# Optimization experiments

Measured on AMD Instinct MI355X. Metric: run time of the kernel, lower is better.

## Reference

```python
import jax, jax.numpy as jnp
import numpy as np

H = 12           # num_heads
D_MODEL = 768
SCALE = (D_MODEL // H) ** -0.5  # qk_scale default: head_dim**-0.5


def _attn_mask(q, k, v, mask):
    # sim: (b, i, j); mask broadcast over query dim (mask.unsqueeze(1) in torch)
    sim = jnp.einsum('bid,bjd->bij', q, k) + mask[:, None, :]
    a = jax.nn.softmax(sim, axis=-1)
    return jnp.einsum('bij,bjd->bid', a, v)


def setup_inputs() -> dict:
    key = jax.random.key(0)
    k0, k1, k2, k3 = jax.random.split(key, 4)
    B, F, n, D = 16, 8, 196, 768
    N = 1 + F * n  # cls + frames*patches = 1569
    x = jax.random.normal(k0, (B, N, D), jnp.float32)
    x_mask = jax.random.normal(k1, (B, N), jnp.float32)  # additive attention mask
    Wqkv = jax.random.normal(k2, (3 * D, D), jnp.float32) * (D ** -0.5)
    Wproj = jax.random.normal(k3, (D, D), jnp.float32) * (D ** -0.5)
    bproj = jnp.zeros((D,), jnp.float32)
    return {"x": x, "x_mask": x_mask, "Wqkv": Wqkv, "Wproj": Wproj,
            "bproj": bproj, "f": F}


def reference(x, x_mask, Wqkv, Wproj, bproj, f):
    B, N, D = x.shape
    h = H
    d = D // h
    # qkv projection (qkv_bias=False), split into q,k,v
    qkv = x @ Wqkv.T                       # (B, N, 3D)
    q, k, v = jnp.split(qkv, 3, axis=-1)

    def to_heads(t):  # 'b n (h d) -> (b h) n d'
        return t.reshape(B, N, h, d).transpose(0, 2, 1, 3).reshape(B * h, N, d)

    q, k, v = map(to_heads, (q, k, v))
    mask = jnp.repeat(x_mask, h, axis=0)   # repeat_interleave over heads: (B*h, N)

    q = q * SCALE
    cls_q, q_ = q[:, :1], q[:, 1:]
    cls_k, k_ = k[:, :1], k[:, 1:]
    cls_v, v_ = v[:, :1], v[:, 1:]
    cls_mask, mask_ = mask[:, :1], mask[:, 1:]

    # cls token attends to everything
    cls_out = _attn_mask(cls_q, k, v, mask)            # (B*h, 1, d)

    # spatial attention: 'b (f n) d -> (b f) n d'
    n = (N - 1) // f
    q_ = q_.reshape(B * h * f, n, d)
    k_ = k_.reshape(B * h * f, n, d)
    v_ = v_.reshape(B * h * f, n, d)
    mask_ = mask_.reshape(B * h * f, n)

    # prepend cls k/v/mask to every frame group (r = f)
    cls_k = jnp.repeat(cls_k, f, axis=0)               # (B*h*f, 1, d)
    cls_v = jnp.repeat(cls_v, f, axis=0)
    cls_m = jnp.repeat(cls_mask, f, axis=0)            # (B*h*f, 1)
    k_ = jnp.concatenate([cls_k, k_], axis=1)          # (B*h*f, n+1, d)
    v_ = jnp.concatenate([cls_v, v_], axis=1)
    m2 = jnp.concatenate([cls_m, mask_], axis=1)       # (B*h*f, n+1)

    out = _attn_mask(q_, k_, v_, m2)                   # (B*h*f, n, d)
    out = out.reshape(B * h, f * n, d)                 # '(b f) n d -> b (f n) d'
    out = jnp.concatenate([cls_out, out], axis=1)      # (B*h, N, d)
    out = out.reshape(B, h, N, d).transpose(0, 2, 1, 3).reshape(B, N, D)
    return out @ Wproj.T + bproj
```

## Files before the change

kernel.cpp:

```cpp
#include <hip/hip_runtime.h>
#include <hip/hip_bf16.h>
#include <stdint.h>

#define Hh 12
#define Dm 768
#define Bb 16
#define Nt 1569
#define Ff 8
#define NC 196
#define BH 192
#define Mr 25104
#define CPW 224
#define VTW (8*CPW)
#define PLD 232
#define CLD 132

typedef __attribute__((ext_vector_type(8))) short bf16x8;
typedef __attribute__((ext_vector_type(4))) float f32x4;

typedef const __attribute__((address_space(1))) uint32_t guint;
typedef __attribute__((address_space(3))) uint32_t luint;

static __device__ __forceinline__ float bf2f(unsigned short u) {
  union { unsigned int i; float f; } v; v.i = ((unsigned int)u) << 16; return v.f;
}
static __device__ __forceinline__ unsigned short f2bf(float f) {
  __hip_bfloat16 h = __float2bfloat16(f);
  return __builtin_bit_cast(unsigned short, h);
}

__global__ void cast_bf16_k(const float4* __restrict__ src, ushort4* __restrict__ dst, int n4) {
  for (int i = blockIdx.x * blockDim.x + threadIdx.x; i < n4; i += gridDim.x * blockDim.x) {
    float4 f = src[i];
    ushort4 u;
    u.x = f2bf(f.x); u.y = f2bf(f.y); u.z = f2bf(f.z); u.w = f2bf(f.w);
    dst[i] = u;
  }
}

template<int MODE>
__global__ __launch_bounds__(256) void gemm_k(
    const __hip_bfloat16* __restrict__ A,
    const __hip_bfloat16* __restrict__ W,
    int M, int K,
    __hip_bfloat16* __restrict__ qh, __hip_bfloat16* __restrict__ kh,
    __hip_bfloat16* __restrict__ vT, __hip_bfloat16* __restrict__ vcls,
    const float* __restrict__ bias, float* __restrict__ outp)
{
  __shared__ __align__(16) unsigned short shmem[128 * CLD];
  unsigned short* ls0 = shmem;
  unsigned short* ls1 = shmem + 4096;
  unsigned short* ls2 = shmem + 8192;
  unsigned short* ls3 = shmem + 12288;

  const int tid = threadIdx.x;
  const int lane = tid & 63, wid = tid >> 6;
  const int waveM = wid >> 1, waveN = wid & 1;

  const int gridN = gridDim.x;
  const int nwg = gridDim.x * gridDim.y;
  int bid = blockIdx.y * gridN + blockIdx.x;
  int q8 = nwg >> 3, r8 = nwg & 7;
  int xcd = bid & 7, lid = bid >> 3;
  int swz = (xcd < r8 ? xcd * (q8 + 1) : r8 * (q8 + 1) + (xcd - r8) * q8) + lid;
  const int mBase = (swz / gridN) * 128, nBase = (swz % gridN) * 128;

  const int l15 = lane & 15, lg = lane >> 4;
  f32x4 acc[4][4] = {};
  const int nkt = K >> 6;
  for (int kt = 0; kt < nkt; ++kt) {
#pragma unroll
    for (int s = 0; s < 2; ++s) {
      int seg = s * 256 + tid;
      int row = seg >> 2, ks = seg & 3;
      int arow = mBase + row; if (arow >= M) arow = M - 1;
      int brow = nBase + row;
      const __hip_bfloat16* ap = A + (size_t)arow * K + kt * 64 + ks * 8;
      const __hip_bfloat16* wp = W + (size_t)brow * K + kt * 64 + ks * 8;
      __builtin_amdgcn_global_load_lds((guint*)ap,        (luint*)&ls0[seg * 8], 16, 0, 0);
      __builtin_amdgcn_global_load_lds((guint*)wp,        (luint*)&ls1[seg * 8], 16, 0, 0);
      __builtin_amdgcn_global_load_lds((guint*)(ap + 32), (luint*)&ls2[seg * 8], 16, 0, 0);
      __builtin_amdgcn_global_load_lds((guint*)(wp + 32), (luint*)&ls3[seg * 8], 16, 0, 0);
    }
    __syncthreads();
    bf16x8 aF[4], bF[4], aG[4], bG[4];
#pragma unroll
    for (int i = 0; i < 4; ++i) {
      int ro = (waveM * 64 + i * 16 + l15) * 32 + lg * 8;
      int co = (waveN * 64 + i * 16 + l15) * 32 + lg * 8;
      aF[i] = *reinterpret_cast<const bf16x8*>(&ls0[ro]);
      bF[i] = *reinterpret_cast<const bf16x8*>(&ls1[co]);
      aG[i] = *reinterpret_cast<const bf16x8*>(&ls2[ro]);
      bG[i] = *reinterpret_cast<const bf16x8*>(&ls3[co]);
    }
#pragma unroll
    for (int mi = 0; mi < 4; ++mi)
#pragma unroll
      for (int ni = 0; ni < 4; ++ni) {
        acc[mi][ni] = __builtin_amdgcn_mfma_f32_16x16x32_bf16(aF[mi], bF[ni], acc[mi][ni], 0, 0, 0);
        acc[mi][ni] = __builtin_amdgcn_mfma_f32_16x16x32_bf16(aG[mi], bG[ni], acc[mi][ni], 0, 0, 0);
      }
    __syncthreads();
  }

  if (MODE == 1) {
    const bool fullM = (mBase + 128 <= M);
#pragma unroll
    for (int mi = 0; mi < 4; ++mi)
#pragma unroll
      for (int ni = 0; ni < 4; ++ni)
#pragma unroll
        for (int r = 0; r < 4; ++r) {
          int grow = mBase + waveM * 64 + mi * 16 + lg * 4 + r;
          if (!fullM && grow >= M) continue;
          int gcol = nBase + waveN * 64 + ni * 16 + l15;
          outp[(size_t)grow * Dm + gcol] = acc[mi][ni][r] + bias[gcol];
        }
    return;
  }

  const int which = nBase / Dm;
  const int headBase = (nBase - which * Dm) >> 6;
  const float scl = (which == 0) ? 0.125f : 1.f;
  const bool fullM = (mBase + 128 <= M);

  if (fullM) {
    if (which < 2) {
#pragma unroll
      for (int mi = 0; mi < 4; ++mi)
#pragma unroll
        for (int ni = 0; ni < 4; ++ni)
#pragma unroll
          for (int r = 0; r < 4; ++r)
            shmem[(waveM * 64 + mi * 16 + lg * 4 + r) * CLD + (waveN * 64 + ni * 16 + l15)]
                = f2bf(acc[mi][ni][r] * scl);
      __syncthreads();
      __hip_bfloat16* dst = (which == 0) ? qh : kh;
      int row = tid >> 1, h = tid & 1;
      int grow = mBase + row;
      int b = grow / Nt, i = grow - b * Nt;
      const uint2* sp = reinterpret_cast<const uint2*>(&shmem[row * CLD + h * 64]);
      uint2* dp = reinterpret_cast<uint2*>(
          dst + ((size_t)(b * Hh + headBase + h) * Nt + i) * 64);
#pragma unroll
      for (int j = 0; j < 16; ++j) dp[j] = sp[j];
    } else {
#pragma unroll
      for (int mi = 0; mi < 4; ++mi)
#pragma unroll
        for (int ni = 0; ni < 4; ++ni)
#pragma unroll
          for (int r = 0; r < 4; ++r)
            shmem[(waveN * 64 + ni * 16 + l15) * CLD + (waveM * 64 + mi * 16 + lg * 4 + r)]
                = f2bf(acc[mi][ni][r]);
      __syncthreads();
      int lc = tid & 127, rhalf = tid >> 7;
      int h = lc >> 6, dc = lc & 63;
      int head = headBase + h;
#pragma unroll
      for (int g = 0; g < 8; ++g) {
        int row0 = rhalf * 64 + g * 8;
        int grow0 = mBase + row0;
        int b = grow0 / Nt, i0 = grow0 - b * Nt;
        const unsigned short* sp = &shmem[lc * CLD + row0];
        if (i0 >= 1 && i0 + 8 <= Nt) {
          int j0 = i0 - 1, cc = j0 / NC, key = j0 - cc * NC;
          if (key + 8 <= NC) {
            int bh = b * Hh + head;
            __hip_bfloat16* p = vT + ((size_t)bh * 64 + dc) * VTW + cc * CPW + key;
            if ((key & 1) == 0) {
              const unsigned int* s4 = reinterpret_cast<const unsigned int*>(sp);
              unsigned int* d4 = reinterpret_cast<unsigned int*>(p);
              d4[0] = s4[0]; d4[1] = s4[1]; d4[2] = s4[2]; d4[3] = s4[3];
            } else {
#pragma unroll
              for (int j = 0; j < 8; ++j)
                p[j] = __builtin_bit_cast(__hip_bfloat16, sp[j]);
            }
            continue;
          }
        }
#pragma unroll
        for (int j = 0; j < 8; ++j) {
          int grow = grow0 + j;
          int bb = grow / Nt, ii = grow - bb * Nt;
          int bh2 = bb * Hh + head;
          unsigned short val = sp[j];
          if (ii == 0) {
            vcls[bh2 * 64 + dc] = __builtin_bit_cast(__hip_bfloat16, val);
          } else {
            int jj = ii - 1, cc2 = jj / NC, k2 = jj - cc2 * NC;
            vT[((size_t)bh2 * 64 + dc) * VTW + cc2 * CPW + k2]
                = __builtin_bit_cast(__hip_bfloat16, val);
          }
        }
      }
    }
  } else {
#pragma unroll
    for (int mi = 0; mi < 4; ++mi)
#pragma unroll
      for (int ni = 0; ni < 4; ++ni)
#pragma unroll
        for (int r = 0; r < 4; ++r) {
          int grow = mBase + waveM * 64 + mi * 16 + lg * 4 + r;
          if (grow >= M) continue;
          int gcol = nBase + waveN * 64 + ni * 16 + l15;
          float v = acc[mi][ni][r];
          int b = grow / Nt, i = grow - b * Nt;
          int hcol = gcol - which * Dm;
          int head = hcol >> 6, dc = hcol & 63;
          int bh = b * Hh + head;
          if (which == 0) {
            qh[((size_t)bh * Nt + i) * 64 + dc] = __float2bfloat16(v * 0.125f);
          } else if (which == 1) {
            kh[((size_t)bh * Nt + i) * 64 + dc] = __float2bfloat16(v);
          } else {
            if (i == 0) vcls[bh * 64 + dc] = __float2bfloat16(v);
            else {
              int j = i - 1; int cc = j / NC, key = j - cc * NC;
              vT[((size_t)bh * 64 + dc) * VTW + cc * CPW + key] = __float2bfloat16(v);
            }
          }
        }
  }
}

__global__ __launch_bounds__(256) void cls_attn_k(
    const __hip_bfloat16* __restrict__ qh, const __hip_bfloat16* __restrict__ kh,
    const __hip_bfloat16* __restrict__ vT, const __hip_bfloat16* __restrict__ vcls,
    const float* __restrict__ x_mask, __hip_bfloat16* __restrict__ ao)
{
  const int bh = blockIdx.x, b = bh / Hh, head = bh - b * Hh;
  const int tid = threadIdx.x;
  __shared__ float sS[Nt];
  __shared__ float qv[64];
  __shared__ float red[256];
  if (tid < 64) qv[tid] = __bfloat162float(qh[((size_t)bh * Nt) * 64 + tid]);
  __syncthreads();
  float lmax = -1e30f;
  for (int j = tid; j < Nt; j += 256) {
    const __hip_bfloat16* kr = kh + ((size_t)bh * Nt + j) * 64;
    float dot = 0.f;
#pragma unroll
    for (int d0 = 0; d0 < 64; d0 += 8) {
      bf16x8 kv = *reinterpret_cast<const bf16x8*>(kr + d0);
#pragma unroll
      for (int i = 0; i < 8; ++i) dot += qv[d0 + i] * bf2f((unsigned short)kv[i]);
    }
    float s = dot + x_mask[b * Nt + j];
    sS[j] = s;
    lmax = fmaxf(lmax, s);
  }
  red[tid] = lmax; __syncthreads();
  for (int off = 128; off > 0; off >>= 1) {
    if (tid < off) red[tid] = fmaxf(red[tid], red[tid + off]);
    __syncthreads();
  }
  float m = red[0]; __syncthreads();
  float lsum = 0.f;
  for (int j = tid; j < Nt; j += 256) { float e = __expf(sS[j] - m); sS[j] = e; lsum += e; }
  red[tid] = lsum; __syncthreads();
  for (int off = 128; off > 0; off >>= 1) {
    if (tid < off) red[tid] += red[tid + off];
    __syncthreads();
  }
  float rden = 1.f / red[0]; __syncthreads();
  int dc = tid & 63, part = tid >> 6;
  float partial = 0.f;
  if (part == 0) partial = sS[0] * __bfloat162float(vcls[bh * 64 + dc]);
  const __hip_bfloat16* vrow = vT + ((size_t)bh * 64 + dc) * VTW;
  for (int cc = part * 2; cc < part * 2 + 2; ++cc) {
    int base = 1 + cc * NC;
    const __hip_bfloat16* vc2 = vrow + cc * CPW;
    int key = 0;
    for (; key + 8 <= NC; key += 8) {
      bf16x8 vv = *reinterpret_cast<const bf16x8*>(vc2 + key);
#pragma unroll
      for (int i = 0; i < 8; ++i)
        partial += sS[base + key + i] * bf2f((unsigned short)vv[i]);
    }
    for (; key < NC; ++key)
      partial += sS[base + key] * __bfloat162float(vc2[key]);
  }
  red[tid] = partial; __syncthreads();
  if (tid < 64) {
    float o = (red[tid] + red[tid + 64] + red[tid + 128] + red[tid + 192]) * rden;
    ao[((size_t)b * Nt) * Dm + head * 64 + dc] = __float2bfloat16(o);
  }
}

__global__ __launch_bounds__(64, 4) void chunk_attn_k(
    const __hip_bfloat16* __restrict__ qh, const __hip_bfloat16* __restrict__ kh,
    const __hip_bfloat16* __restrict__ vT, const __hip_bfloat16* __restrict__ vcls,
    const float* __restrict__ x_mask, __hip_bfloat16* __restrict__ ao)
{
  const int bid = blockIdx.x;
  const int work = (bid & 7) * 2496 + (bid >> 3);
  const int g = work / 13;
  const int rtile = work - g * 13;
  const int bh = g >> 3, c = g & 7;
  const int b = bh / Hh, head = bh - b * Hh;
  const int lane = threadIdx.x;
  const int l15 = lane & 15, lg = lane >> 4;
  __shared__ __align__(16) __hip_bfloat16 ldsP[16 * PLD];

  int qlrow = rtile * 16 + l15;
  int qtok = 1 + c * NC + qlrow; if (qtok > Nt - 1) qtok = Nt - 1;
  const __hip_bfloat16* qp = qh + ((size_t)bh * Nt + qtok) * 64;
  bf16x8 aQ0 = *reinterpret_cast<const bf16x8*>(qp + lg * 8);
  bf16x8 aQ1 = *reinterpret_cast<const bf16x8*>(qp + 32 + lg * 8);

  float pc0;
  {
    const __hip_bfloat16* kc = kh + (size_t)bh * Nt * 64;
    bf16x8 ck0 = *reinterpret_cast<const bf16x8*>(kc + lg * 8);
    bf16x8 ck1 = *reinterpret_cast<const bf16x8*>(kc + 32 + lg * 8);
    float p = 0.f;
#pragma unroll
    for (int i = 0; i < 8; ++i)
      p += bf2f((unsigned short)aQ0[i]) * bf2f((unsigned short)ck0[i])
         + bf2f((unsigned short)aQ1[i]) * bf2f((unsigned short)ck1[i]);
    p += __shfl_xor(p, 16);
    p += __shfl_xor(p, 32);
    pc0 = p + x_mask[b * Nt];
  }

  f32x4 S[13];
#pragma unroll 2
  for (int nt = 0; nt < 13; ++nt) {
    int key = nt * 16 + l15;
    int ktok = 1 + c * NC + key; if (ktok > Nt - 1) ktok = Nt - 1;
    const __hip_bfloat16* kp = kh + ((size_t)bh * Nt + ktok) * 64;
    bf16x8 b0 = *reinterpret_cast<const bf16x8*>(kp + lg * 8);
    bf16x8 b1 = *reinterpret_cast<const bf16x8*>(kp + 32 + lg * 8);
    f32x4 sa = {};
    sa = __builtin_amdgcn_mfma_f32_16x16x32_bf16(aQ0, b0, sa, 0, 0, 0);
    sa = __builtin_amdgcn_mfma_f32_16x16x32_bf16(aQ1, b1, sa, 0, 0, 0);
    float mv = (key < NC) ? x_mask[b * Nt + 1 + c * NC + key] : -1e30f;
#pragma unroll
    for (int r = 0; r < 4; ++r) S[nt][r] = sa[r] + mv;
  }

  float pcls[4], rden[4];
#pragma unroll
  for (int r = 0; r < 4; ++r) {
    float m = -1e30f;
#pragma unroll
    for (int nt = 0; nt < 13; ++nt) m = fmaxf(m, S[nt][r]);
    m = fmaxf(m, __shfl_xor(m, 1));
    m = fmaxf(m, __shfl_xor(m, 2));
    m = fmaxf(m, __shfl_xor(m, 4));
    m = fmaxf(m, __shfl_xor(m, 8));
    float sc = __shfl(pc0, lg * 4 + r);
    m = fmaxf(m, sc);
    float sum = 0.f;
#pragma unroll
    for (int nt = 0; nt < 13; ++nt) { float e = __expf(S[nt][r] - m); S[nt][r] = e; sum += e; }
    sum += __shfl_xor(sum, 1);
    sum += __shfl_xor(sum, 2);
    sum += __shfl_xor(sum, 4);
    sum += __shfl_xor(sum, 8);
    float pc = __expf(sc - m);
    pcls[r] = pc;
    rden[r] = 1.f / (sum + pc);
  }

#pragma unroll
  for (int nt = 0; nt < 13; ++nt)
#pragma unroll
    for (int r = 0; r < 4; ++r)
      ldsP[(lg * 4 + r) * PLD + nt * 16 + l15] = __float2bfloat16(S[nt][r]);
#pragma unroll
  for (int r = 0; r < 4; ++r)
    ldsP[l15 * PLD + 208 + lg * 4 + r] = __float2bfloat16(0.f);
  __syncthreads();

  f32x4 O[4] = {};
#pragma unroll
  for (int kt = 0; kt < 7; ++kt) {
    bf16x8 aP = *reinterpret_cast<const bf16x8*>(&ldsP[l15 * PLD + kt * 32 + lg * 8]);
#pragma unroll
    for (int ni = 0; ni < 4; ++ni) {
      int dc = ni * 16 + l15;
      bf16x8 bV = *reinterpret_cast<const bf16x8*>(
          vT + ((size_t)bh * 64 + dc) * VTW + c * CPW + kt * 32 + lg * 8);
      O[ni] = __builtin_amdgcn_mfma_f32_16x16x32_bf16(aP, bV, O[ni], 0, 0, 0);
    }
  }
#pragma unroll
  for (int ni = 0; ni < 4; ++ni) {
    int dc = ni * 16 + l15;
    float vc = __bfloat162float(vcls[bh * 64 + dc]);
#pragma unroll
    for (int r = 0; r < 4; ++r) {
      int lrow = rtile * 16 + lg * 4 + r;
      if (lrow < NC) {
        float o = (O[ni][r] + pcls[r] * vc) * rden[r];
        int tok = 1 + c * NC + lrow;
        ao[((size_t)b * Nt + tok) * Dm + head * 64 + dc] = __float2bfloat16(o);
      }
    }
  }
}

extern "C" void kernel_launch(void* const* d_in, const int* in_sizes, int n_in,
                              void* d_out, int out_size, void* d_ws, size_t ws_size,
                              hipStream_t stream) {
  const float* x     = (const float*)d_in[0];
  const float* xmask = (const float*)d_in[1];
  const float* wqkv  = (const float*)d_in[2];
  const float* wproj = (const float*)d_in[3];
  const float* bproj = (const float*)d_in[4];
  float* outp = (float*)d_out;

  char* ws = (char*)d_ws;
  size_t off = 0;
  auto alloc = [&](size_t bytes) {
    char* p = ws + off;
    off += (bytes + 255) & ~(size_t)255;
    return p;
  };
  __hip_bfloat16* xb     = (__hip_bfloat16*)alloc((size_t)Mr * Dm * 2);
  __hip_bfloat16* wqkvb  = (__hip_bfloat16*)alloc((size_t)3 * Dm * Dm * 2);
  __hip_bfloat16* wprojb = (__hip_bfloat16*)alloc((size_t)Dm * Dm * 2);
  __hip_bfloat16* qh     = (__hip_bfloat16*)alloc((size_t)BH * Nt * 64 * 2);
  __hip_bfloat16* kh     = (__hip_bfloat16*)alloc((size_t)BH * Nt * 64 * 2);
  __hip_bfloat16* vT     = (__hip_bfloat16*)alloc((size_t)BH * 64 * VTW * 2);
  __hip_bfloat16* vcls   = (__hip_bfloat16*)alloc((size_t)BH * 64 * 2);
  __hip_bfloat16* ao = xb;

  cast_bf16_k<<<2048, 256, 0, stream>>>((const float4*)x, (ushort4*)xb, Mr * Dm / 4);
  cast_bf16_k<<<512, 256, 0, stream>>>((const float4*)wqkv, (ushort4*)wqkvb, 3 * Dm * Dm / 4);
  cast_bf16_k<<<256, 256, 0, stream>>>((const float4*)wproj, (ushort4*)wprojb, Dm * Dm / 4);

  gemm_k<0><<<dim3(18, 197), 256, 0, stream>>>(xb, wqkvb, Mr, Dm, qh, kh, vT, vcls, nullptr, nullptr);

  cls_attn_k<<<BH, 256, 0, stream>>>(qh, kh, vT, vcls, xmask, ao);
  chunk_attn_k<<<13 * BH * Ff, 64, 0, stream>>>(qh, kh, vT, vcls, xmask, ao);

  gemm_k<1><<<dim3(6, 197), 256, 0, stream>>>(ao, wprojb, Mr, Dm, nullptr, nullptr, nullptr, nullptr, bproj, outp);
}
```

Baseline: 375.0 us.

## Double-buffer GEMM LDS tiles to overlap global loads with MFMA

Splits the GEMM K-loop into 32-wide steps and alternates between two LDS buffers. The next tile is prefetched via global_load_lds while MFMAs run on the current tile, so only one barrier per step is needed. The goal is to hide global-memory latency that previously sat serialized before each compute phase. The trade-off is half as much MFMA work per barrier and more loop iterations, and the overlap depends on how the compiler places waitcnt before the barrier.

```diff
diff --git a/kernel.cpp b/kernel.cpp
--- a/kernel.cpp
+++ b/kernel.cpp
@@ -48,10 +48,6 @@
     const float* __restrict__ bias, float* __restrict__ outp)
 {
   __shared__ __align__(16) unsigned short shmem[128 * CLD];
-  unsigned short* ls0 = shmem;
-  unsigned short* ls1 = shmem + 4096;
-  unsigned short* ls2 = shmem + 8192;
-  unsigned short* ls3 = shmem + 12288;
 
   const int tid = threadIdx.x;
   const int lane = tid & 63, wid = tid >> 6;
@@ -66,41 +62,51 @@
   const int mBase = (swz / gridN) * 128, nBase = (swz % gridN) * 128;
 
   const int l15 = lane & 15, lg = lane >> 4;
+
+  int arow0, brow0, ks0, arow1, brow1, ks1;
+  {
+    int seg = tid;
+    int row = seg >> 2; ks0 = seg & 3;
+    arow0 = mBase + row; if (arow0 >= M) arow0 = M - 1;
+    brow0 = nBase + row;
+    seg = 256 + tid;
+    row = seg >> 2; ks1 = seg & 3;
+    arow1 = mBase + row; if (arow1 >= M) arow1 = M - 1;
+    brow1 = nBase + row;
+  }
+  auto STAGE = [&](int half, int kt) {
+    const __hip_bfloat16* a0 = A + (size_t)arow0 * K + kt * 32 + ks0 * 8;
+    const __hip_bfloat16* w0 = W + (size_t)brow0 * K + kt * 32 + ks0 * 8;
+    const __hip_bfloat16* a1 = A + (size_t)arow1 * K + kt * 32 + ks1 * 8;
+    const __hip_bfloat16* w1 = W + (size_t)brow1 * K + kt * 32 + ks1 * 8;
+    unsigned short* base = shmem + half * 8192;
+    __builtin_amdgcn_global_load_lds((guint*)a0, (luint*)&base[tid * 8], 16, 0, 0);
+    __builtin_amdgcn_global_load_lds((guint*)w0, (luint*)&base[4096 + tid * 8], 16, 0, 0);
+    __builtin_amdgcn_global_load_lds((guint*)a1, (luint*)&base[(256 + tid) * 8], 16, 0, 0);
+    __builtin_amdgcn_global_load_lds((guint*)w1, (luint*)&base[4096 + (256 + tid) * 8], 16, 0, 0);
+  };
+
   f32x4 acc[4][4] = {};
-  const int nkt = K >> 6;
+  const int nkt = K >> 5;
+  int cur = 0;
+  STAGE(0, 0);
+  __syncthreads();
   for (int kt = 0; kt < nkt; ++kt) {
-#pragma unroll
-    for (int s = 0; s < 2; ++s) {
-      int seg = s * 256 + tid;
-      int row = seg >> 2, ks = seg & 3;
-      int arow = mBase + row; if (arow >= M) arow = M - 1;
-      int brow = nBase + row;
-      const __hip_bfloat16* ap = A + (size_t)arow * K + kt * 64 + ks * 8;
-      const __hip_bfloat16* wp = W + (size_t)brow * K + kt * 64 + ks * 8;
-      __builtin_amdgcn_global_load_lds((guint*)ap,        (luint*)&ls0[seg * 8], 16, 0, 0);
-      __builtin_amdgcn_global_load_lds((guint*)wp,        (luint*)&ls1[seg * 8], 16, 0, 0);
-      __builtin_amdgcn_global_load_lds((guint*)(ap + 32), (luint*)&ls2[seg * 8], 16, 0, 0);
-      __builtin_amdgcn_global_load_lds((guint*)(wp + 32), (luint*)&ls3[seg * 8], 16, 0, 0);
-    }
+    if (kt + 1 < nkt) STAGE(cur ^ 1, kt + 1);
+    const unsigned short* base = shmem + cur * 8192;
+    bf16x8 aF[4], bF[4];
+#pragma unroll
+    for (int i = 0; i < 4; ++i) {
+      aF[i] = *reinterpret_cast<const bf16x8*>(&base[(waveM * 64 + i * 16 + l15) * 32 + lg * 8]);
+      bF[i] = *reinterpret_cast<const bf16x8*>(&base[4096 + (waveN * 64 + i * 16 + l15) * 32 + lg * 8]);
+    }
+#pragma unroll
+    for (int mi = 0; mi < 4; ++mi)
+#pragma unroll
+      for (int ni = 0; ni < 4; ++ni)
+        acc[mi][ni] = __builtin_amdgcn_mfma_f32_16x16x32_bf16(aF[mi], bF[ni], acc[mi][ni], 0, 0, 0);
     __syncthreads();
-    bf16x8 aF[4], bF[4], aG[4], bG[4];
-#pragma unroll
-    for (int i = 0; i < 4; ++i) {
-      int ro = (waveM * 64 + i * 16 + l15) * 32 + lg * 8;
-      int co = (waveN * 64 + i * 16 + l15) * 32 + lg * 8;
-      aF[i] = *reinterpret_cast<const bf16x8*>(&ls0[ro]);
-      bF[i] = *reinterpret_cast<const bf16x8*>(&ls1[co]);
-      aG[i] = *reinterpret_cast<const bf16x8*>(&ls2[ro]);
-      bG[i] = *reinterpret_cast<const bf16x8*>(&ls3[co]);
-    }
-#pragma unroll
-    for (int mi = 0; mi < 4; ++mi)
-#pragma unroll
-      for (int ni = 0; ni < 4; ++ni) {
-        acc[mi][ni] = __builtin_amdgcn_mfma_f32_16x16x32_bf16(aF[mi], bF[ni], acc[mi][ni], 0, 0, 0);
-        acc[mi][ni] = __builtin_amdgcn_mfma_f32_16x16x32_bf16(aG[mi], bG[ni], acc[mi][ni], 0, 0, 0);
-      }
-    __syncthreads();
+    cur ^= 1;
   }
 
   if (MODE == 1) {
```

Result: slower. 383.2 us (+2.2%).
